# Performance work log

Measured on AMD Instinct MI355X. Metric: run time of the kernel, lower is better.

The kernel has to match this reference:

```python
import jax, jax.numpy as jnp
import numpy as np
from jax import lax

GAMMA = 2.0
BLANK = 0
NEG = -1e30  # log-space 'zero'
T, B, C, L = 1000, 64, 256, 100


def setup_inputs() -> dict:
    key = jax.random.key(0)
    k1, k2 = jax.random.split(key)
    # valid log-probabilities, as produced by a model's log_softmax head
    log_probs = jax.nn.log_softmax(jax.random.normal(k1, (T, B, C), dtype=jnp.float32), axis=-1)
    # concatenated targets, blank (0) excluded as CTC requires
    targets = jax.random.randint(k2, (B * L,), 1, C, dtype=jnp.int32)
    input_lengths = jnp.full((B,), T, dtype=jnp.int32)
    target_lengths = jnp.full((B,), L, dtype=jnp.int32)
    return {"log_probs": log_probs, "targets": targets,
            "input_lengths": input_lengths, "target_lengths": target_lengths}


def _ctc_loss(log_probs, targets2d, input_lengths, target_lengths):
    # log_probs: (T,B,C); targets2d: (B,L). Returns per-sample NLL (B,).
    Tt, Bb, _ = log_probs.shape
    Ll = targets2d.shape[1]
    S = 2 * Ll + 1  # extended label sequence: blank interleaved
    ext = jnp.full((Bb, S), BLANK, dtype=jnp.int32).at[:, 1::2].set(targets2d)
    # emission log-probs for each extended symbol: (T,B,S)
    emit = jnp.take_along_axis(log_probs, jnp.broadcast_to(ext[None], (Tt, Bb, S)), axis=2)
    # skip-transition allowed where symbol is non-blank and differs from s-2
    allow2 = jnp.concatenate(
        [jnp.zeros((Bb, 2), bool), (ext[:, 2:] != BLANK) & (ext[:, 2:] != ext[:, :-2])], axis=1)

    def shiftk(a, k):
        return jnp.pad(a, ((0, 0), (k, 0)), constant_values=NEG)[:, :S]

    alpha0 = jnp.full((Bb, S), NEG, jnp.float32).at[:, 0].set(emit[0, :, 0]).at[:, 1].set(emit[0, :, 1])

    def step(alpha, e):
        a1 = shiftk(alpha, 1)
        a2 = jnp.where(allow2, shiftk(alpha, 2), NEG)
        m = jnp.maximum(jnp.maximum(alpha, a1), a2)
        new = m + jnp.log(jnp.exp(alpha - m) + jnp.exp(a1 - m) + jnp.exp(a2 - m)) + e
        return new, new

    _, rest = lax.scan(step, alpha0, emit[1:])
    alphas = jnp.concatenate([alpha0[None], rest], axis=0)  # (T,B,S)
    b = jnp.arange(Bb)
    last = alphas[input_lengths - 1, b]  # (B,S) at each sample's final step
    ll = jnp.logaddexp(last[b, 2 * target_lengths], last[b, 2 * target_lengths - 1])
    # zero_infinity=True semantics
    return jnp.where(ll > NEG / 2, -ll, 0.0)


def reference(log_probs, targets, input_lengths, target_lengths):
    targets2d = targets.reshape(B, L)
    loss = _ctc_loss(log_probs, targets2d, input_lengths, target_lengths)  # (B,)
    # focal weights: mean-over-time prob of each target symbol (computed under no_grad in torch)
    mean_probs = jnp.exp(log_probs).mean(axis=0)  # (B,C)
    target_probs = lax.stop_gradient(
        jnp.take_along_axis(mean_probs, targets2d, axis=1).reshape(-1))  # (B*L,)
    focal_weight = (1.0 - target_probs) ** GAMMA
    # torch broadcasting quirk: (total,) * (B,1) -> (B,total); mean over all
    return (focal_weight[None, :] * loss[:, None]).mean()
```

## Files before the change

kernel.cpp:

```cpp
#include <hip/hip_runtime.h>
#include <cstdint>

#define T_DIM 1000
#define B_DIM 64
#define C_DIM 256
#define L_DIM 100
#define S_DIM (2 * L_DIM + 1)
#define CH 16
#define MEAN_SLICES 8
#define MEAN_ROWS (T_DIM / MEAN_SLICES)

#define DPP_I(x, ctrl) __builtin_amdgcn_update_dpp(0, (x), (ctrl), 0xF, 0xF, true)
#define DPP_F(x, ctrl) __int_as_float(DPP_I(__float_as_int(x), (ctrl)))

__device__ __forceinline__ float wave_max_dpp(float x) {
    x = fmaxf(x, DPP_F(x, 0x111));
    x = fmaxf(x, DPP_F(x, 0x112));
    x = fmaxf(x, DPP_F(x, 0x114));
    x = fmaxf(x, DPP_F(x, 0x118));
    x = fmaxf(x, DPP_F(x, 0x142));
    x = fmaxf(x, DPP_F(x, 0x143));
    return __int_as_float(__builtin_amdgcn_readlane(__float_as_int(x), 63));
}

__global__ __launch_bounds__(256, 1) void ctc_fused(
        const float* __restrict__ lp,
        const int* __restrict__ tgt,
        const int* __restrict__ il,
        const int* __restrict__ tl,
        float* __restrict__ ws_mean,
        float* __restrict__ ws_loss) {
    const int blk = blockIdx.x;
    const uint32_t rstride = B_DIM * C_DIM;

    if (blk >= B_DIM) {
        const int mb = blk - B_DIM;
        const int b = mb >> 3;
        const int slice = mb & 7;
        const int c = threadIdx.x;
        const float* p = lp + (size_t)b * C_DIM + c + (size_t)(slice * MEAN_ROWS) * rstride;
        float s0 = 0.f, s1 = 0.f, s2 = 0.f, s3 = 0.f, s4 = 0.f;
        for (int t = 0; t < MEAN_ROWS; t += 5) {
            s0 += __expf(p[(size_t)(t + 0) * rstride]);
            s1 += __expf(p[(size_t)(t + 1) * rstride]);
            s2 += __expf(p[(size_t)(t + 2) * rstride]);
            s3 += __expf(p[(size_t)(t + 3) * rstride]);
            s4 += __expf(p[(size_t)(t + 4) * rstride]);
        }
        atomicAdd(&ws_mean[b * C_DIM + c], (s0 + s1 + s2 + s3 + s4) * (1.0f / T_DIM));
        return;
    }

    if (threadIdx.x >= 64) return;
    const int b = blk;
    const int lane = threadIdx.x;
    const int* trow = tgt + b * L_DIM;
    const int ilen = il[b];
    const int tlen = tl[b];

    const int i1 = 2 * lane;
    const int i3 = 2 * lane + 1;
    const int c1 = (i1 < L_DIM) ? trow[i1] : 0;
    const int c3 = (i3 < L_DIM) ? trow[i3] : 0;
    const int c1m = (i1 >= 1 && i1 - 1 < L_DIM) ? trow[i1 - 1] : -1;
    const float m1 = ((i1 >= 1) && (c1 != c1m)) ? 1.0f : 0.0f;
    const float m3 = (c3 != c1) ? 1.0f : 0.0f;

    const float f0 = (4 * lane + 0 < S_DIM) ? 1.0f : 0.0f;
    const float f1 = (4 * lane + 1 < S_DIM) ? 1.0f : 0.0f;
    const float f2 = (4 * lane + 2 < S_DIM) ? 1.0f : 0.0f;
    const float f3 = (4 * lane + 3 < S_DIM) ? 1.0f : 0.0f;

    const float* base = lp + (size_t)b * C_DIM;

    float a0 = 0.f, a1 = 0.f, a2 = 0.f, a3 = 0.f;
    {
        float i0 = __expf(base[0]);
        float i1v = __expf(base[c1]);
        if (lane == 0) { a0 = i0; a1 = i1v; }
    }
    float ls = 0.f;

#define RENORM() do {                                                       \
        a0 *= f0; a1 *= f1; a2 *= f2; a3 *= f3;                             \
        const float mx = wave_max_dpp(fmaxf(fmaxf(a0, a1), fmaxf(a2, a3))); \
        const float inv = __builtin_amdgcn_rcpf(mx);                        \
        ls -= __logf(inv);                                                  \
        a0 *= inv; a1 *= inv; a2 *= inv; a3 *= inv;                         \
    } while (0)

    float Ab[CH], A1[CH], A3[CH], Bb[CH], B1[CH], B3[CH];

    auto burst = [&](float* vb, float* v1, float* v3, int tstart) {
#pragma unroll
        for (int d = 0; d < CH; ++d) {
            int tp = tstart + d; tp = (tp < ilen) ? tp : (ilen - 1);
            const uint32_t ro = (uint32_t)tp * rstride;
            vb[d] = base[ro];
            v1[d] = base[ro + (uint32_t)c1];
            v3[d] = base[ro + (uint32_t)c3];
        }
    };

    auto step = [&](float lb, float l1, float l3) {
        const float pb  = __expf(lb);
        const float p1e = __expf(l1);
        const float p3e = __expf(l3);
        const float p3 = DPP_F(a3, 0x138);
        const float a01 = a0 + a1;
        const float n0 = (a0 + p3) * pb;
        const float n1 = fmaf(m1, p3, a01) * p1e;
        const float n2 = (a2 + a1) * pb;
        const float n3 = (fmaf(m3, a1, a2) + a3) * p3e;
        a0 = n0; a1 = n1; a2 = n2; a3 = n3;
    };

    auto chunk16 = [&](const float* vb, const float* v1, const float* v3) {
#pragma unroll
        for (int d = 0; d < CH; ++d) {
            step(vb[d], v1[d], v3[d]);
            if ((d & 7) == 7) RENORM();
        }
    };

    burst(Ab, A1, A3, 1);
    burst(Bb, B1, B3, 1 + CH);

    int t = 1;
    for (; t + 2 * CH <= ilen; t += 2 * CH) {
        chunk16(Ab, A1, A3);
        burst(Ab, A1, A3, t + 2 * CH);
        chunk16(Bb, B1, B3);
        burst(Bb, B1, B3, t + 3 * CH);
    }

#pragma unroll
    for (int d = 0; d < CH; ++d) {
        const int tt = t + d;
        if (tt < ilen) {
            step(Ab[d], A1[d], A3[d]);
            if ((d & 7) == 7) RENORM();
        }
    }
#pragma unroll
    for (int d = 0; d < CH; ++d) {
        const int tt = t + CH + d;
        if (tt < ilen) {
            step(Bb[d], B1[d], B3[d]);
            if ((d & 7) == 7) RENORM();
        }
    }
#undef RENORM

    const int s_hi = 2 * tlen;
    const int s_lo = 2 * tlen - 1;
    const int slot_hi = s_hi & 3, lane_hi = min(s_hi >> 2, 63);
    const int slot_lo = s_lo & 3, lane_lo = min(s_lo >> 2, 63);
    float ch = (slot_hi == 0) ? a0 : (slot_hi == 1) ? a1 : (slot_hi == 2) ? a2 : a3;
    float cl = (slot_lo == 0) ? a0 : (slot_lo == 1) ? a1 : (slot_lo == 2) ? a2 : a3;
    const float vh = __shfl(ch, lane_hi, 64);
    const float vl = __shfl(cl, lane_lo, 64);
    if (lane == 0) {
        const float s = vh + vl;
        const float loss = (s > 0.f) ? -(__logf(s) + ls) : 0.0f;
        ws_loss[b] = loss;
    }
}

__global__ __launch_bounds__(256) void ctc_finalize(
        const float* __restrict__ ws_mean, const float* __restrict__ ws_loss,
        const int* __restrict__ tgt, float* __restrict__ out) {
    const int tid = threadIdx.x;
    float fsum = 0.f;
#pragma unroll
    for (int k = 0; k < (B_DIM * L_DIM) / 256; ++k) {
        const int j = tid + k * 256;
        const int b = j / L_DIM;
        const int c = tgt[j];
        const float p = ws_mean[b * C_DIM + c];
        const float w = 1.0f - p;
        fsum += w * w;
    }
    float lsum = (tid < B_DIM) ? ws_loss[tid] : 0.f;
#pragma unroll
    for (int off = 32; off > 0; off >>= 1) {
        fsum += __shfl_down(fsum, off, 64);
        lsum += __shfl_down(lsum, off, 64);
    }
    __shared__ float sf[4], sl[4];
    const int w = tid >> 6;
    if ((tid & 63) == 0) { sf[w] = fsum; sl[w] = lsum; }
    __syncthreads();
    if (tid == 0) {
        const float F = sf[0] + sf[1] + sf[2] + sf[3];
        const float Lo = sl[0] + sl[1] + sl[2] + sl[3];
        out[0] = (F / (float)(B_DIM * L_DIM)) * (Lo / (float)B_DIM);
    }
}

extern "C" void kernel_launch(void* const* d_in, const int* in_sizes, int n_in,
                              void* d_out, int out_size, void* d_ws, size_t ws_size,
                              hipStream_t stream) {
    const float* lp = (const float*)d_in[0];
    const int* tgt = (const int*)d_in[1];
    const int* il = (const int*)d_in[2];
    const int* tl = (const int*)d_in[3];
    float* ws_mean = (float*)d_ws;
    float* ws_loss = ws_mean + B_DIM * C_DIM;

    hipMemsetAsync(ws_mean, 0, B_DIM * C_DIM * sizeof(float), stream);
    ctc_fused<<<dim3(B_DIM + MEAN_SLICES * B_DIM), dim3(256), 0, stream>>>(
        lp, tgt, il, tl, ws_mean, ws_loss);
    ctc_finalize<<<dim3(1), dim3(256), 0, stream>>>(ws_mean, ws_loss, tgt, (float*)d_out);
}
```

Measured before the change: 166.7 us.

## Use producer waves to stage emissions in LDS for the CTC recurrence wave

Instead of one wave loading its own register double-buffered bursts of emission log-probs, three extra waves in each CTC block gather the blank and target emissions for the next 16 timesteps into a double-buffered shared-memory ring. The single consumer wave reads from LDS and runs the serial recurrence, with a block barrier after every chunk. The goal is to take global-load latency and register pressure off the critical serial wave. In exchange it adds a __syncthreads per 16 steps and LDS reads inside the dependent chain, and the producer wave's loads for one chunk may not finish before the barrier.

```diff
diff --git a/kernel.cpp b/kernel.cpp
--- a/kernel.cpp
+++ b/kernel.cpp
@@ -51,9 +51,12 @@
         return;
     }
 
-    if (threadIdx.x >= 64) return;
+    __shared__ float buf[2][CH][3][64];
+
+    const int tid = threadIdx.x;
+    const int lane = tid & 63;
+    const int wave = tid >> 6;
     const int b = blk;
-    const int lane = threadIdx.x;
     const int* trow = tgt + b * L_DIM;
     const int ilen = il[b];
     const int tlen = tl[b];
@@ -81,24 +84,28 @@
     }
     float ls = 0.f;
 
-#define RENORM() do {                                                       \
-        a0 *= f0; a1 *= f1; a2 *= f2; a3 *= f3;                             \
-        const float mx = wave_max_dpp(fmaxf(fmaxf(a0, a1), fmaxf(a2, a3))); \
-        const float inv = __builtin_amdgcn_rcpf(mx);                        \
-        ls -= __logf(inv);                                                  \
-        a0 *= inv; a1 *= inv; a2 *= inv; a3 *= inv;                         \
-    } while (0)
-
-    float Ab[CH], A1[CH], A3[CH], Bb[CH], B1[CH], B3[CH];
-
-    auto burst = [&](float* vb, float* v1, float* v3, int tstart) {
-#pragma unroll
-        for (int d = 0; d < CH; ++d) {
-            int tp = tstart + d; tp = (tp < ilen) ? tp : (ilen - 1);
-            const uint32_t ro = (uint32_t)tp * rstride;
-            vb[d] = base[ro];
-            v1[d] = base[ro + (uint32_t)c1];
-            v3[d] = base[ro + (uint32_t)c3];
+    const int nchunks = (ilen - 1 + CH - 1) / CH;
+
+    auto produce = [&](int cc, int p) {
+        const int tstart = 1 + cc * CH;
+        float Lb[6], L1v[6], L3v[6];
+#pragma unroll
+        for (int k = 0; k < 6; ++k) {
+            const int d = (wave - 1) + 3 * k;
+            if (d < CH) {
+                int t = tstart + d; t = (t < ilen) ? t : (ilen - 1);
+                const float* r = base + (size_t)t * rstride;
+                Lb[k] = r[0]; L1v[k] = r[c1]; L3v[k] = r[c3];
+            }
+        }
+#pragma unroll
+        for (int k = 0; k < 6; ++k) {
+            const int d = (wave - 1) + 3 * k;
+            if (d < CH) {
+                buf[p][d][0][lane] = Lb[k];
+                buf[p][d][1][lane] = L1v[k];
+                buf[p][d][2][lane] = L3v[k];
+            }
         }
     };
 
@@ -115,42 +122,44 @@
         a0 = n0; a1 = n1; a2 = n2; a3 = n3;
     };
 
-    auto chunk16 = [&](const float* vb, const float* v1, const float* v3) {
-#pragma unroll
-        for (int d = 0; d < CH; ++d) {
-            step(vb[d], v1[d], v3[d]);
-            if ((d & 7) == 7) RENORM();
+#define RENORM() do {                                                       \
+        a0 *= f0; a1 *= f1; a2 *= f2; a3 *= f3;                             \
+        const float mx = wave_max_dpp(fmaxf(fmaxf(a0, a1), fmaxf(a2, a3))); \
+        const float inv = __builtin_amdgcn_rcpf(mx);                        \
+        ls -= __logf(inv);                                                  \
+        a0 *= inv; a1 *= inv; a2 *= inv; a3 *= inv;                         \
+    } while (0)
+
+    auto consume = [&](int cc) {
+        const int p = cc & 1;
+        const int tstart = 1 + cc * CH;
+        if (tstart + CH <= ilen) {
+#pragma unroll
+            for (int d = 0; d < CH; ++d) {
+                step(buf[p][d][0][lane], buf[p][d][1][lane], buf[p][d][2][lane]);
+                if ((d & 7) == 7) RENORM();
+            }
+        } else {
+#pragma unroll
+            for (int d = 0; d < CH; ++d) {
+                if (tstart + d < ilen) {
+                    step(buf[p][d][0][lane], buf[p][d][1][lane], buf[p][d][2][lane]);
+                    if ((d & 7) == 7) RENORM();
+                }
+            }
         }
     };
 
-    burst(Ab, A1, A3, 1);
-    burst(Bb, B1, B3, 1 + CH);
-
-    int t = 1;
-    for (; t + 2 * CH <= ilen; t += 2 * CH) {
-        chunk16(Ab, A1, A3);
-        burst(Ab, A1, A3, t + 2 * CH);
-        chunk16(Bb, B1, B3);
-        burst(Bb, B1, B3, t + 3 * CH);
-    }
-
-#pragma unroll
-    for (int d = 0; d < CH; ++d) {
-        const int tt = t + d;
-        if (tt < ilen) {
-            step(Ab[d], A1[d], A3[d]);
-            if ((d & 7) == 7) RENORM();
-        }
-    }
-#pragma unroll
-    for (int d = 0; d < CH; ++d) {
-        const int tt = t + CH + d;
-        if (tt < ilen) {
-            step(Bb[d], B1[d], B3[d]);
-            if ((d & 7) == 7) RENORM();
-        }
+    if (wave != 0) produce(0, 0);
+    __syncthreads();
+    for (int c = 0; c < nchunks; ++c) {
+        if (wave != 0) produce(c + 1, (c + 1) & 1);
+        else consume(c);
+        __syncthreads();
     }
 #undef RENORM
+
+    if (wave != 0) return;
 
     const int s_hi = 2 * tlen;
     const int s_lo = 2 * tlen - 1;
```

New measurement: 167.2 us. Within noise of the previous version (+0.2%).
